# Kernel optimization log

Hardware: AMD Instinct MI355X
Metric: run time of the kernel (lower is better)

The kernel has to match this reference:

```python
import jax, jax.numpy as jnp
import numpy as np

B, T, C, H = 2, 2048, 1024, 16
HD = C // H  # head_size = 64


def setup_inputs() -> dict:
    key = jax.random.key(0)
    ks = jax.random.split(key, 5)
    s_in = 1.0 / np.sqrt(C)
    x = jax.random.normal(ks[0], (B, T, C), dtype=jnp.float32)
    # per-head bias-free Q/K/V projections, stacked over heads: [H, C, HD]
    Wq = jax.random.normal(ks[1], (H, C, HD), dtype=jnp.float32) * s_in
    Wk = jax.random.normal(ks[2], (H, C, HD), dtype=jnp.float32) * s_in
    Wv = jax.random.normal(ks[3], (H, C, HD), dtype=jnp.float32) * s_in
    # output projection with bias: [C, C], [C]
    Wo = jax.random.normal(ks[4], (C, C), dtype=jnp.float32) * s_in
    bo = jnp.zeros((C,), dtype=jnp.float32)
    return {"x": x, "Wq": Wq, "Wk": Wk, "Wv": Wv, "Wo": Wo, "bo": bo}


def reference(x, Wq, Wk, Wv, Wo, bo):
    # Per-head projections (equivalent to the per-head Linear loop, batched)
    q = jnp.einsum('btc,hcd->bhtd', x, Wq)  # [B,H,T,HD]
    k = jnp.einsum('btc,hcd->bhtd', x, Wk)
    v = jnp.einsum('btc,hcd->bhtd', x, Wv)
    scale = 1.0 / jnp.sqrt(jnp.asarray(HD, dtype=x.dtype))
    scores = jnp.einsum('bhtd,bhsd->bhts', q, k) * scale  # [B,H,T,T]
    causal = jnp.tril(jnp.ones((T, T), dtype=bool))
    scores = jnp.where(causal, scores, jnp.asarray(-jnp.inf, dtype=scores.dtype))
    attn = jax.nn.softmax(scores, axis=-1)
    out = jnp.einsum('bhts,bhsd->bhtd', attn, v)  # [B,H,T,HD]
    # concat heads back to [B,T,C] (head order matches torch.cat over heads)
    out = out.transpose(0, 2, 1, 3).reshape(B, T, C)
    y = out @ Wo.T + bo  # output projection (dropout=0 in eval)
    return y
```

## Files before the change

### kernel.cpp

```cpp
#include <hip/hip_runtime.h>
#include <hip/hip_bf16.h>


typedef __attribute__((ext_vector_type(8))) short  short8;
typedef __attribute__((ext_vector_type(4))) float  f32x4;
typedef __attribute__((ext_vector_type(4))) unsigned short ushort4v;

#define MFMA16(a, b, c) __builtin_amdgcn_mfma_f32_16x16x32_bf16((a), (b), (c), 0, 0, 0)
#define LOG2E 1.4426950408889634f

__device__ __forceinline__ unsigned short f2bf(float f) {
    __hip_bfloat16 h = __float2bfloat16(f);
    return __builtin_bit_cast(unsigned short, h);
}

typedef __attribute__((address_space(1))) const unsigned int gu32_t;
typedef __attribute__((address_space(3))) unsigned int lu32_t;
__device__ __forceinline__ void gload16(const void* g, void* l) {
    __builtin_amdgcn_global_load_lds((gu32_t*)g, (lu32_t*)l, 16, 0, 0);
}


__global__ __launch_bounds__(256) void cvt_f32_bf16(const float* __restrict__ src,
                                                    unsigned short* __restrict__ dst, int n4) {
    int i = blockIdx.x * blockDim.x + threadIdx.x;
    int stride = gridDim.x * blockDim.x;
    for (; i < n4; i += stride) {
        f32x4 v = *reinterpret_cast<const f32x4*>(src + (size_t)i * 4);
        ushort4v o;
        o.x = f2bf(v.x); o.y = f2bf(v.y); o.z = f2bf(v.z); o.w = f2bf(v.w);
        *reinterpret_cast<ushort4v*>(dst + (size_t)i * 4) = o;
    }
}

__global__ __launch_bounds__(256) void cvt_w_t(const float* __restrict__ Wq,
                                               const float* __restrict__ Wk,
                                               const float* __restrict__ Wv,
                                               unsigned short* __restrict__ Wt) {
    const float* W = (blockIdx.z == 0) ? Wq : ((blockIdx.z == 1) ? Wk : Wv);
    const float scale = (blockIdx.z == 0) ? 0.125f : 1.0f;
    __shared__ unsigned short lT[64][65];
    const int h = blockIdx.y, c0 = blockIdx.x * 64;
    const int tid = threadIdx.x;
#pragma unroll
    for (int p = 0; p < 16; ++p) {
        int e = tid + p * 256;
        int i = e >> 6, d = e & 63;
        float v = W[((size_t)(h * 1024 + c0 + i)) * 64 + d];
        lT[d][i] = f2bf(v * scale);
    }
    __syncthreads();
    unsigned short* outp = Wt + ((size_t)blockIdx.z << 20);
#pragma unroll
    for (int p = 0; p < 16; ++p) {
        int e = tid + p * 256;
        int d = e >> 6, j = e & 63;
        outp[(size_t)(h * 64 + d) * 1024 + c0 + j] = lT[d][j];
    }
}


__device__ __forceinline__ void gemm_mainloop(const unsigned short* __restrict__ A,
                                              const unsigned short* __restrict__ Bm,
                                              int Kd, int m0, int n0,
                                              short* lA, short* lB, f32x4 acc[4][4]) {
    const int tid = threadIdx.x;
    const int lane = tid & 63;
    const int w = tid >> 6, wr = w >> 1, wc = w & 1;
    for (int k0 = 0; k0 < Kd; k0 += 64) {
        __syncthreads();
#pragma unroll
        for (int pp = 0; pp < 4; ++pp) {
            int n = tid + pp * 256;
            int row = n >> 3;
            int cc = (n & 7) ^ (row & 7);
            gload16(A + (size_t)(m0 + row) * Kd + k0 + cc * 8, lA + n * 8);
            gload16(Bm + (size_t)(n0 + row) * Kd + k0 + cc * 8, lB + n * 8);
        }
        __syncthreads();
#pragma unroll
        for (int kk = 0; kk < 2; ++kk) {
            short8 aF[4], bF[4];
#pragma unroll
            for (int mi = 0; mi < 4; ++mi) {
                int r = wr * 64 + mi * 16 + (lane & 15);
                int c = kk * 4 + (lane >> 4);
                aF[mi] = *reinterpret_cast<const short8*>(lA + r * 64 + ((c ^ (r & 7)) << 3));
            }
#pragma unroll
            for (int ni = 0; ni < 4; ++ni) {
                int r = wc * 64 + ni * 16 + (lane & 15);
                int c = kk * 4 + (lane >> 4);
                bF[ni] = *reinterpret_cast<const short8*>(lB + r * 64 + ((c ^ (r & 7)) << 3));
            }
#pragma unroll
            for (int mi = 0; mi < 4; ++mi)
#pragma unroll
                for (int ni = 0; ni < 4; ++ni)
                    acc[mi][ni] = MFMA16(aF[mi], bF[ni], acc[mi][ni]);
        }
    }
}

__global__ __launch_bounds__(256) void gemm_qkv(const unsigned short* __restrict__ A,
                                                const unsigned short* __restrict__ Bm,
                                                unsigned short* __restrict__ Qb,
                                                unsigned short* __restrict__ Kb,
                                                unsigned short* __restrict__ Vt) {
    __shared__ alignas(16) short lA[128 * 64], lB[128 * 64];
    f32x4 acc[4][4];
#pragma unroll
    for (int i = 0; i < 4; ++i)
#pragma unroll
        for (int j = 0; j < 4; ++j) acc[i][j] = (f32x4){0.f, 0.f, 0.f, 0.f};
    const int m0 = blockIdx.y * 128, n0 = blockIdx.x * 128;
    gemm_mainloop(A, Bm, 1024, m0, n0, lA, lB, acc);

    const int lane = threadIdx.x & 63;
    const int w = threadIdx.x >> 6, wr = w >> 1, wc = w & 1;
#pragma unroll
    for (int mi = 0; mi < 4; ++mi)
#pragma unroll
        for (int ni = 0; ni < 4; ++ni) {
            int col = n0 + wc * 64 + ni * 16 + (lane & 15);
            int t = col >> 10, hd = col & 1023;
            int h = hd >> 6, d = hd & 63;
#pragma unroll
            for (int r = 0; r < 4; ++r) {
                int row = m0 + wr * 64 + mi * 16 + (lane >> 4) * 4 + r;
                int b = row >> 11, tt = row & 2047;
                int bh = b * 16 + h;
                unsigned short val = f2bf(acc[mi][ni][r]);
                if (t == 0) {
                    Qb[(((size_t)bh * 2048 + tt) << 6) + d] = val;
                } else if (t == 1) {
                    Kb[(((size_t)bh * 2048 + tt) << 6) + d] = val;
                } else {
                    int c = tt & 63;
                    int cp = (c & 32) | (((c >> 2) & 3) << 3) | (((c >> 4) & 1) << 2) | (c & 3);
                    int fc = ((((cp >> 3) ^ (d & 7)) & 7) << 3) | (cp & 7);
                    Vt[(size_t)bh * 131072 + (size_t)d * 2048 + (tt & ~63) + fc] = val;
                }
            }
        }
}

__global__ __launch_bounds__(256) void gemm_out(const unsigned short* __restrict__ A,
                                                const unsigned short* __restrict__ Bm,
                                                const float* __restrict__ bo,
                                                float* __restrict__ Y) {
    __shared__ alignas(16) short lA[128 * 64], lB[128 * 64];
    f32x4 acc[4][4];
#pragma unroll
    for (int i = 0; i < 4; ++i)
#pragma unroll
        for (int j = 0; j < 4; ++j) acc[i][j] = (f32x4){0.f, 0.f, 0.f, 0.f};
    const int m0 = blockIdx.y * 128, n0 = blockIdx.x * 128;
    gemm_mainloop(A, Bm, 1024, m0, n0, lA, lB, acc);

    const int lane = threadIdx.x & 63;
    const int w = threadIdx.x >> 6, wr = w >> 1, wc = w & 1;
#pragma unroll
    for (int mi = 0; mi < 4; ++mi)
#pragma unroll
        for (int ni = 0; ni < 4; ++ni) {
            int col = n0 + wc * 64 + ni * 16 + (lane & 15);
            float bv = bo[col];
#pragma unroll
            for (int r = 0; r < 4; ++r) {
                int row = m0 + wr * 64 + mi * 16 + (lane >> 4) * 4 + r;
                Y[(size_t)row * 1024 + col] = acc[mi][ni][r] + bv;
            }
        }
}


__global__ __launch_bounds__(256, 2) void attn_kernel(const unsigned short* __restrict__ Q,
                                                      const unsigned short* __restrict__ K,
                                                      const unsigned short* __restrict__ Vt,
                                                      unsigned short* __restrict__ AO) {
    __shared__ alignas(16) short lK[2][64 * 64];
    __shared__ alignas(16) short lV[2][64 * 64];

    const int tid = threadIdx.x, lane = tid & 63, w = tid >> 6;
    const int ql = lane & 15, g = lane >> 4;
    const int p = blockIdx.x, bh = blockIdx.y;
    const int qtA = p, qtB = 31 - p, NT = 32 - p;
    const size_t base = (size_t)bh * 2048 * 64;
    const unsigned short* Vg = Vt + (size_t)bh * 131072;
    const int qAb = qtA * 64 + w * 16, qBb = qtB * 64 + w * 16;

    short8 qfA[2], qfB[2];
#pragma unroll
    for (int kk = 0; kk < 2; ++kk) {
        qfA[kk] = *reinterpret_cast<const short8*>(&Q[base + (size_t)(qAb + ql) * 64 + kk * 32 + g * 8]);
        qfB[kk] = *reinterpret_cast<const short8*>(&Q[base + (size_t)(qBb + ql) * 64 + kk * 32 + g * 8]);
    }

    f32x4 oA[4], oB[4];
#pragma unroll
    for (int dt = 0; dt < 4; ++dt) { oA[dt] = (f32x4){0.f,0.f,0.f,0.f}; oB[dt] = (f32x4){0.f,0.f,0.f,0.f}; }
    float mA = -1e30f, sumA = 0.f, mB = -1e30f, sumB = 0.f;

    auto stage = [&](int buf, int kv0) {
        const unsigned short* Kg = K + base + (size_t)kv0 * 64;
        short* dK = &lK[buf][0];
        short* dV = &lV[buf][0];
#pragma unroll
        for (int pp = 0; pp < 2; ++pp) {
            int n = tid + pp * 256;
            gload16(Kg + (size_t)(n >> 3) * 64 + (((n & 7) ^ ((n >> 3) & 7)) << 3), dK + n * 8);
            gload16(Vg + (size_t)(n >> 3) * 2048 + kv0 + ((n & 7) << 3), dV + n * 8);
        }
    };

    stage(0, 0);
    __syncthreads();

    const short* cK;
    const short* cV;

    auto process = [&](const short8* qf, f32x4* o, float& m, float& sum, int qb, int kv0, bool diag) {
        f32x4 s[4];
#pragma unroll
        for (int ct = 0; ct < 4; ++ct) s[ct] = (f32x4){0.f, 0.f, 0.f, 0.f};
#pragma unroll
        for (int kk = 0; kk < 2; ++kk)
#pragma unroll
            for (int ct = 0; ct < 4; ++ct) {
                int r = ct * 16 + ql;
                short8 kf = *reinterpret_cast<const short8*>(
                    cK + r * 64 + (((kk * 4 + g) ^ (r & 7)) << 3));
                s[ct] = MFMA16(kf, qf[kk], s[ct]);
            }
        if (diag) {
            int q = qb + ql;
#pragma unroll
            for (int ct = 0; ct < 4; ++ct)
#pragma unroll
                for (int r = 0; r < 4; ++r)
                    if (kv0 + ct * 16 + g * 4 + r > q) s[ct][r] = -1e30f;
        }
        float tm = s[0][0];
#pragma unroll
        for (int ct = 0; ct < 4; ++ct)
#pragma unroll
            for (int r = 0; r < 4; ++r) tm = fmaxf(tm, s[ct][r]);
        tm = fmaxf(tm, __shfl_xor(tm, 16));
        tm = fmaxf(tm, __shfl_xor(tm, 32));
        float mn = fmaxf(m, tm);
        float al = __builtin_amdgcn_exp2f((m - mn) * LOG2E);
        float rs = 0.f;
#pragma unroll
        for (int ct = 0; ct < 4; ++ct)
#pragma unroll
            for (int r = 0; r < 4; ++r) {
                float pv = __builtin_amdgcn_exp2f((s[ct][r] - mn) * LOG2E);
                s[ct][r] = pv;
                rs += pv;
            }
        rs += __shfl_xor(rs, 16);
        rs += __shfl_xor(rs, 32);
        sum = al * sum + rs;
        m = mn;
        short8 pa[2];
#pragma unroll
        for (int kt = 0; kt < 2; ++kt)
#pragma unroll
            for (int j = 0; j < 8; ++j)
                pa[kt][j] = (short)f2bf(s[kt * 2 + (j >> 2)][j & 3]);
#pragma unroll
        for (int r = 0; r < 4; ++r) {
            float ar = __shfl(al, (lane & 48) | (g * 4 + r));
            o[0][r] *= ar; o[1][r] *= ar; o[2][r] *= ar; o[3][r] *= ar;
        }
#pragma unroll
        for (int dt = 0; dt < 4; ++dt) {
            int d = dt * 16 + ql;
#pragma unroll
            for (int kt = 0; kt < 2; ++kt) {
                short8 vf = *reinterpret_cast<const short8*>(
                    cV + d * 64 + ((((kt * 4 + g) ^ (d & 7)) & 7) << 3));
                o[dt] = MFMA16(pa[kt], vf, o[dt]);
            }
        }
    };

    for (int i = 0; i < NT; ++i) {
        const int cur = i & 1;
        if (i + 1 < NT) stage(cur ^ 1, (i + 1) * 64);
        const int kv0 = i * 64;
        cK = &lK[cur][0];
        cV = &lV[cur][0];

        process(qfB, oB, mB, sumB, qBb, kv0, i == NT - 1);
        if (i <= p) process(qfA, oA, mA, sumA, qAb, kv0, i == p);

        __syncthreads();
    }

    const int b = bh >> 4, h = bh & 15;
    auto epi = [&](f32x4* o, float sum, int qb) {
#pragma unroll
        for (int r = 0; r < 4; ++r) {
            float li = __shfl(sum, (lane & 48) | (g * 4 + r));
            float inv = 1.0f / li;
            int q = qb + g * 4 + r;
#pragma unroll
            for (int dt = 0; dt < 4; ++dt) {
                int d = dt * 16 + ql;
                AO[((size_t)(b * 2048 + q) << 10) + h * 64 + d] = f2bf(o[dt][r] * inv);
            }
        }
    };
    epi(oA, sumA, qAb);
    epi(oB, sumB, qBb);
}


extern "C" void kernel_launch(void* const* d_in, const int* in_sizes, int n_in,
                              void* d_out, int out_size, void* d_ws, size_t ws_size,
                              hipStream_t stream) {
    const float* x  = (const float*)d_in[0];
    const float* Wq = (const float*)d_in[1];
    const float* Wk = (const float*)d_in[2];
    const float* Wv = (const float*)d_in[3];
    const float* Wo = (const float*)d_in[4];
    const float* bo = (const float*)d_in[5];
    float* y = (float*)d_out;

    char* ws = (char*)d_ws;
    unsigned short* xb  = (unsigned short*)(ws);
    unsigned short* Wt  = (unsigned short*)(ws + ((size_t)8  << 20));
    unsigned short* Wob = (unsigned short*)(ws + ((size_t)14 << 20));
    unsigned short* Qb  = (unsigned short*)(ws + ((size_t)16 << 20));
    unsigned short* Kb  = (unsigned short*)(ws + ((size_t)24 << 20));
    unsigned short* Vt  = (unsigned short*)(ws + ((size_t)32 << 20));
    unsigned short* AO  = (unsigned short*)(ws + ((size_t)40 << 20));

    cvt_f32_bf16<<<2048, 256, 0, stream>>>(x, xb, 4096 * 1024 / 4);
    cvt_f32_bf16<<<1024, 256, 0, stream>>>(Wo, Wob, 1024 * 1024 / 4);
    cvt_w_t<<<dim3(16, 16, 3), 256, 0, stream>>>(Wq, Wk, Wv, Wt);
    gemm_qkv<<<dim3(24, 32), 256, 0, stream>>>(xb, Wt, Qb, Kb, Vt);
    attn_kernel<<<dim3(16, 32), 256, 0, stream>>>(Qb, Kb, Vt, AO);
    gemm_out<<<dim3(8, 32), 256, 0, stream>>>(AO, Wob, bo, y);
}
```

Measured before the change: 203.2 us.

## Template GEMM mainloop, use 8-wave blocks, smaller out-proj tiles, setprio around MFMAs

The GEMM mainloop becomes a template over block and warp geometry. The QKV GEMM now runs 8 waves per 128x128 tile and the output GEMM uses 128x64 tiles with 8 waves, which doubles its grid to fill more CUs. Each wave holds fewer accumulators, so occupancy can rise. The attention kernel also raises wave priority around its MFMA sections with s_setprio so other waves' softmax work can interleave. The cost is more waves sharing each tile's LDS bandwidth, plus twice as many global reloads of A in the output GEMM.

```diff
diff --git a/kernel.cpp b/kernel.cpp
--- a/kernel.cpp
+++ b/kernel.cpp
@@ -60,74 +60,80 @@
 }
 
 
+template<int BM, int BN, int WM, int WN, int FM, int FN>
 __device__ __forceinline__ void gemm_mainloop(const unsigned short* __restrict__ A,
                                               const unsigned short* __restrict__ Bm,
                                               int Kd, int m0, int n0,
-                                              short* lA, short* lB, f32x4 acc[4][4]) {
+                                              short* lA, short* lB, f32x4 (&acc)[FM][FN]) {
+    static_assert(BM == WM * FM * 16 && BN == WN * FN * 16, "geometry");
+    constexpr int THREADS = WM * WN * 64;
     const int tid = threadIdx.x;
-    const int lane = tid & 63;
-    const int w = tid >> 6, wr = w >> 1, wc = w & 1;
+    const int lane = tid & 63, ql = lane & 15, g = lane >> 4;
+    const int w = tid >> 6, wr = w / WN, wc = w % WN;
     for (int k0 = 0; k0 < Kd; k0 += 64) {
         __syncthreads();
 #pragma unroll
-        for (int pp = 0; pp < 4; ++pp) {
-            int n = tid + pp * 256;
+        for (int n = tid; n < BM * 8; n += THREADS) {
             int row = n >> 3;
             int cc = (n & 7) ^ (row & 7);
             gload16(A + (size_t)(m0 + row) * Kd + k0 + cc * 8, lA + n * 8);
+        }
+#pragma unroll
+        for (int n = tid; n < BN * 8; n += THREADS) {
+            int row = n >> 3;
+            int cc = (n & 7) ^ (row & 7);
             gload16(Bm + (size_t)(n0 + row) * Kd + k0 + cc * 8, lB + n * 8);
         }
         __syncthreads();
 #pragma unroll
         for (int kk = 0; kk < 2; ++kk) {
-            short8 aF[4], bF[4];
-#pragma unroll
-            for (int mi = 0; mi < 4; ++mi) {
-                int r = wr * 64 + mi * 16 + (lane & 15);
-                int c = kk * 4 + (lane >> 4);
+            short8 aF[FM], bF[FN];
+            int c = kk * 4 + g;
+#pragma unroll
+            for (int mi = 0; mi < FM; ++mi) {
+                int r = wr * (FM * 16) + mi * 16 + ql;
                 aF[mi] = *reinterpret_cast<const short8*>(lA + r * 64 + ((c ^ (r & 7)) << 3));
             }
 #pragma unroll
-            for (int ni = 0; ni < 4; ++ni) {
-                int r = wc * 64 + ni * 16 + (lane & 15);
-                int c = kk * 4 + (lane >> 4);
+            for (int ni = 0; ni < FN; ++ni) {
+                int r = wc * (FN * 16) + ni * 16 + ql;
                 bF[ni] = *reinterpret_cast<const short8*>(lB + r * 64 + ((c ^ (r & 7)) << 3));
             }
 #pragma unroll
-            for (int mi = 0; mi < 4; ++mi)
-#pragma unroll
-                for (int ni = 0; ni < 4; ++ni)
+            for (int mi = 0; mi < FM; ++mi)
+#pragma unroll
+                for (int ni = 0; ni < FN; ++ni)
                     acc[mi][ni] = MFMA16(aF[mi], bF[ni], acc[mi][ni]);
         }
     }
 }
 
-__global__ __launch_bounds__(256) void gemm_qkv(const unsigned short* __restrict__ A,
-                                                const unsigned short* __restrict__ Bm,
-                                                unsigned short* __restrict__ Qb,
-                                                unsigned short* __restrict__ Kb,
-                                                unsigned short* __restrict__ Vt) {
+__global__ __launch_bounds__(512, 4) void gemm_qkv(const unsigned short* __restrict__ A,
+                                                   const unsigned short* __restrict__ Bm,
+                                                   unsigned short* __restrict__ Qb,
+                                                   unsigned short* __restrict__ Kb,
+                                                   unsigned short* __restrict__ Vt) {
     __shared__ alignas(16) short lA[128 * 64], lB[128 * 64];
-    f32x4 acc[4][4];
+    f32x4 acc[4][2];
 #pragma unroll
     for (int i = 0; i < 4; ++i)
 #pragma unroll
-        for (int j = 0; j < 4; ++j) acc[i][j] = (f32x4){0.f, 0.f, 0.f, 0.f};
+        for (int j = 0; j < 2; ++j) acc[i][j] = (f32x4){0.f, 0.f, 0.f, 0.f};
     const int m0 = blockIdx.y * 128, n0 = blockIdx.x * 128;
-    gemm_mainloop(A, Bm, 1024, m0, n0, lA, lB, acc);
-
-    const int lane = threadIdx.x & 63;
-    const int w = threadIdx.x >> 6, wr = w >> 1, wc = w & 1;
+    gemm_mainloop<128, 128, 2, 4, 4, 2>(A, Bm, 1024, m0, n0, lA, lB, acc);
+
+    const int lane = threadIdx.x & 63, ql = lane & 15, g = lane >> 4;
+    const int w = threadIdx.x >> 6, wr = w / 4, wc = w % 4;
 #pragma unroll
     for (int mi = 0; mi < 4; ++mi)
 #pragma unroll
-        for (int ni = 0; ni < 4; ++ni) {
-            int col = n0 + wc * 64 + ni * 16 + (lane & 15);
+        for (int ni = 0; ni < 2; ++ni) {
+            int col = n0 + wc * 32 + ni * 16 + ql;
             int t = col >> 10, hd = col & 1023;
             int h = hd >> 6, d = hd & 63;
 #pragma unroll
             for (int r = 0; r < 4; ++r) {
-                int row = m0 + wr * 64 + mi * 16 + (lane >> 4) * 4 + r;
+                int row = m0 + wr * 64 + mi * 16 + g * 4 + r;
                 int b = row >> 11, tt = row & 2047;
                 int bh = b * 16 + h;
                 unsigned short val = f2bf(acc[mi][ni][r]);
@@ -145,30 +151,30 @@
         }
 }
 
-__global__ __launch_bounds__(256) void gemm_out(const unsigned short* __restrict__ A,
-                                                const unsigned short* __restrict__ Bm,
-                                                const float* __restrict__ bo,
-                                                float* __restrict__ Y) {
-    __shared__ alignas(16) short lA[128 * 64], lB[128 * 64];
-    f32x4 acc[4][4];
-#pragma unroll
-    for (int i = 0; i < 4; ++i)
-#pragma unroll
-        for (int j = 0; j < 4; ++j) acc[i][j] = (f32x4){0.f, 0.f, 0.f, 0.f};
-    const int m0 = blockIdx.y * 128, n0 = blockIdx.x * 128;
-    gemm_mainloop(A, Bm, 1024, m0, n0, lA, lB, acc);
-
-    const int lane = threadIdx.x & 63;
-    const int w = threadIdx.x >> 6, wr = w >> 1, wc = w & 1;
-#pragma unroll
-    for (int mi = 0; mi < 4; ++mi)
-#pragma unroll
-        for (int ni = 0; ni < 4; ++ni) {
-            int col = n0 + wc * 64 + ni * 16 + (lane & 15);
+__global__ __launch_bounds__(512, 4) void gemm_out(const unsigned short* __restrict__ A,
+                                                   const unsigned short* __restrict__ Bm,
+                                                   const float* __restrict__ bo,
+                                                   float* __restrict__ Y) {
+    __shared__ alignas(16) short lA[128 * 64], lB[64 * 64];
+    f32x4 acc[2][2];
+#pragma unroll
+    for (int i = 0; i < 2; ++i)
+#pragma unroll
+        for (int j = 0; j < 2; ++j) acc[i][j] = (f32x4){0.f, 0.f, 0.f, 0.f};
+    const int m0 = blockIdx.y * 128, n0 = blockIdx.x * 64;
+    gemm_mainloop<128, 64, 4, 2, 2, 2>(A, Bm, 1024, m0, n0, lA, lB, acc);
+
+    const int lane = threadIdx.x & 63, ql = lane & 15, g = lane >> 4;
+    const int w = threadIdx.x >> 6, wr = w / 2, wc = w % 2;
+#pragma unroll
+    for (int mi = 0; mi < 2; ++mi)
+#pragma unroll
+        for (int ni = 0; ni < 2; ++ni) {
+            int col = n0 + wc * 32 + ni * 16 + ql;
             float bv = bo[col];
 #pragma unroll
             for (int r = 0; r < 4; ++r) {
-                int row = m0 + wr * 64 + mi * 16 + (lane >> 4) * 4 + r;
+                int row = m0 + wr * 32 + mi * 16 + g * 4 + r;
                 Y[(size_t)row * 1024 + col] = acc[mi][ni][r] + bv;
             }
         }
@@ -224,6 +230,7 @@
         f32x4 s[4];
 #pragma unroll
         for (int ct = 0; ct < 4; ++ct) s[ct] = (f32x4){0.f, 0.f, 0.f, 0.f};
+        __builtin_amdgcn_s_setprio(1);
 #pragma unroll
         for (int kk = 0; kk < 2; ++kk)
 #pragma unroll
@@ -233,6 +240,7 @@
                     cK + r * 64 + (((kk * 4 + g) ^ (r & 7)) << 3));
                 s[ct] = MFMA16(kf, qf[kk], s[ct]);
             }
+        __builtin_amdgcn_s_setprio(0);
         if (diag) {
             int q = qb + ql;
 #pragma unroll
@@ -274,6 +282,7 @@
             float ar = __shfl(al, (lane & 48) | (g * 4 + r));
             o[0][r] *= ar; o[1][r] *= ar; o[2][r] *= ar; o[3][r] *= ar;
         }
+        __builtin_amdgcn_s_setprio(1);
 #pragma unroll
         for (int dt = 0; dt < 4; ++dt) {
             int d = dt * 16 + ql;
@@ -284,6 +293,7 @@
                 o[dt] = MFMA16(pa[kt], vf, o[dt]);
             }
         }
+        __builtin_amdgcn_s_setprio(0);
     };
 
     for (int i = 0; i < NT; ++i) {
@@ -341,7 +351,7 @@
     cvt_f32_bf16<<<2048, 256, 0, stream>>>(x, xb, 4096 * 1024 / 4);
     cvt_f32_bf16<<<1024, 256, 0, stream>>>(Wo, Wob, 1024 * 1024 / 4);
     cvt_w_t<<<dim3(16, 16, 3), 256, 0, stream>>>(Wq, Wk, Wv, Wt);
-    gemm_qkv<<<dim3(24, 32), 256, 0, stream>>>(xb, Wt, Qb, Kb, Vt);
+    gemm_qkv<<<dim3(24, 32), 512, 0, stream>>>(xb, Wt, Qb, Kb, Vt);
     attn_kernel<<<dim3(16, 32), 256, 0, stream>>>(Qb, Kb, Vt, AO);
-    gemm_out<<<dim3(8, 32), 256, 0, stream>>>(AO, Wob, bo, y);
-}
+    gemm_out<<<dim3(16, 32), 512, 0, stream>>>(AO, Wob, bo, y);
+}
```

Result: faster. 191.3 us (-5.8%).
